# Performance work log

Hardware: AMD Instinct MI355X
Metric: run time of the kernel (lower is better)

Reference implementation:

```python
import jax, jax.numpy as jnp
import numpy as np

LAYERS = [3, 256, 256, 256, 256, 256, 256, 3]
W_BC, W_DIV, W_JXB = 1.0, 1.0, 1.0  # weight1 = [1.0, 1.0, 1.0]


def setup_inputs() -> dict:
    key = jax.random.key(0)
    ks = jax.random.split(key, 32)
    N0, NF = 16384, 32768
    inp = {
        "x0": jax.random.uniform(ks[0], (N0, 1), jnp.float32),
        "y0": jax.random.uniform(ks[1], (N0, 1), jnp.float32),
        "bx0": jax.random.normal(ks[2], (N0, 1), jnp.float32),
        "by0": jax.random.normal(ks[3], (N0, 1), jnp.float32),
        "bz0": jax.random.normal(ks[4], (N0, 1), jnp.float32),
        "xyz_f": jax.random.uniform(ks[5], (NF, 3), jnp.float32),
        "lb": jnp.zeros((3,), jnp.float32),
        "ub": jnp.ones((3,), jnp.float32),
    }
    # Xavier-normal weights, zero biases (as in initialize_NN)
    for l in range(len(LAYERS) - 1):
        fan_in, fan_out = LAYERS[l], LAYERS[l + 1]
        std = (2.0 / (fan_in + fan_out)) ** 0.5
        inp[f"W{l}"] = std * jax.random.normal(ks[6 + l], (fan_in, fan_out), jnp.float32)
        inp[f"b{l}"] = jnp.zeros((1, fan_out), jnp.float32)
    return inp


def reference(x0, y0, bx0, by0, bz0, xyz_f, lb, ub,
              W0, b0, W1, b1, W2, b2, W3, b3, W4, b4, W5, b5, W6, b6):
    Ws = [W0, W1, W2, W3, W4, W5, W6]
    bs = [b0, b1, b2, b3, b4, b5, b6]

    def net(p):  # p: (3,) -> (3,) field [bx, by, bz]
        h = 2.0 * (p - lb) / (ub - lb) - 1.0
        for W, b in zip(Ws[:-1], bs[:-1]):
            h = jnp.tanh(h @ W + b[0])
        return h @ Ws[-1] + bs[-1][0]

    # Boundary term at z = 0
    pts0 = jnp.concatenate([x0, y0, jnp.zeros_like(x0)], axis=1)  # (N0, 3)
    b_bc = jax.vmap(net)(pts0)  # (N0, 3)

    # One fused forward-mode pass gives the full 3x3 Jacobian + primal,
    # replacing the 9 separate autograd.grad sweeps of the torch code.
    def val_and_jac(p):
        primal, jac = jax.vmap(lambda t: jax.jvp(net, (p,), (t,)))(jnp.eye(3, dtype=p.dtype))
        return primal[0], jac  # jac[j, i] = d b_i / d x_j

    bf, jac = jax.vmap(val_and_jac)(xyz_f)  # (NF, 3), (NF, 3, 3)

    div = jac[:, 0, 0] + jac[:, 1, 1] + jac[:, 2, 2]  # bx_x + by_y + bz_z
    bx, by, bz = bf[:, 0], bf[:, 1], bf[:, 2]
    jx = jac[:, 1, 2] - jac[:, 2, 1]  # bz_y - by_z
    jy = jac[:, 2, 0] - jac[:, 0, 2]  # bx_z - bz_x
    jz = jac[:, 0, 1] - jac[:, 1, 0]  # by_x - bx_y
    jxb = (jy * bz - jz * by) ** 2 + (jz * bx - jx * bz) ** 2 + (jx * by - jy * bx) ** 2

    loss = (W_BC * jnp.mean((b_bc[:, 0:1] - bx0) ** 2)
            + W_BC * jnp.mean((b_bc[:, 1:2] - by0) ** 2)
            + W_BC * jnp.mean((b_bc[:, 2:3] - bz0) ** 2)
            + W_DIV * jnp.mean(div ** 2)
            + W_JXB * jnp.mean(jxb))
    return loss
```

## Files before the change

### kernel.cpp

```cpp
#include <hip/hip_runtime.h>
#include <math.h>

typedef short bf16x8 __attribute__((ext_vector_type(8)));
typedef float f32x4 __attribute__((ext_vector_type(4)));

#define NPT0 16384
#define NPTF 32768

__device__ __forceinline__ short f2b(float f) {
  union { float f; unsigned u; } v; v.f = f;
  return (short)((v.u + 0x7FFFu + ((v.u >> 16) & 1u)) >> 16);
}
__device__ __forceinline__ int cvtpk(float a, float b) {
  int r;
  asm("v_cvt_pk_bf16_f32 %0, %1, %2" : "=v"(r) : "v"(a), "v"(b));
  return r;
}
__device__ __forceinline__ float tanh_fast(float z) {
  const float e = __expf(2.f * z);
  return 1.f - 2.f * __builtin_amdgcn_rcpf(e + 1.f);
}
__device__ __forceinline__ int inplane(int n, int c) {
  return ((n >> 5) << 9) + ((((n >> 3) & 3) * 16 + c) << 3) + (n & 7);
}

__global__ void prep_kernel(const float* __restrict__ W1, const float* __restrict__ W2,
                            const float* __restrict__ W3, const float* __restrict__ W4,
                            const float* __restrict__ W5, const float* __restrict__ W6,
                            short* __restrict__ Wt)
{
  const int i = blockIdx.x * 256 + threadIdx.x;
  if (i < 5 * 65536) {
    const int layer = i >> 16;
    const float* src = layer == 0 ? W1 : layer == 1 ? W2 : layer == 2 ? W3
                     : layer == 3 ? W4 : W5;
    const int w  = i & 65535;
    const int nt = w >> 12;
    const int ks = (w >> 9) & 7;
    const int l  = (w >> 3) & 63;
    const int e  = w & 7;
    const int n  = nt * 16 + (l & 15);
    const int k  = ks * 32 + (l >> 4) * 8 + e;
    Wt[i] = f2b(src[k * 256 + n]);
  } else {
    const int w  = i - 5 * 65536;
    const int ks = w >> 9;
    const int l  = (w >> 3) & 63;
    const int e  = w & 7;
    const int n  = l & 15;
    const int k  = ks * 32 + (l >> 4) * 8 + e;
    Wt[i] = (n < 3) ? f2b(W6[k * 3 + n]) : (short)0;
  }
}

__global__ __launch_bounds__(512, 4) void field_kernel(
    const float* __restrict__ xyz_f,
    const float* __restrict__ lb, const float* __restrict__ ub,
    const float* __restrict__ W0, const float* __restrict__ b0,
    const float* __restrict__ b1, const float* __restrict__ b2,
    const float* __restrict__ b3, const float* __restrict__ b4,
    const float* __restrict__ b5,
    const short* __restrict__ Wt,
    const float* __restrict__ b6,
    float* __restrict__ part_div2, float* __restrict__ part_jxb)
{
  __shared__ short act[4 * 8192];
  __shared__ float redD[4 * 96];
  const int tid = threadIdx.x;
  const int lane = tid & 63;
  const int wv = tid >> 6;
  const int c = lane & 15;
  const int kg = lane >> 4;

  const float lbx = lb[0], lby = lb[1], lbz = lb[2];
  const float sx = 2.f / (ub[0] - lbx);
  const float sy = 2.f / (ub[1] - lby);
  const float sz = 2.f / (ub[2] - lbz);

  {
    const int pp = tid & 15;
    const int pg = (tid >> 4) & 1;
    const int pt = blockIdx.x * 32 + pg * 16 + pp;
    const int n0 = (tid >> 5) * 16;
    const float hx = (xyz_f[pt * 3 + 0] - lbx) * sx - 1.f;
    const float hy = (xyz_f[pt * 3 + 1] - lby) * sy - 1.f;
    const float hz = (xyz_f[pt * 3 + 2] - lbz) * sz - 1.f;
    float th[16], vx[16], vy[16], vz[16];
#pragma unroll
    for (int j = 0; j < 16; ++j) {
      const int n = n0 + j;
      const float w0 = W0[n], w1 = W0[256 + n], w2 = W0[512 + n];
      const float z = b0[n] + hx * w0 + hy * w1 + hz * w2;
      const float t = tanh_fast(z);
      const float g = 1.f - t * t;
      th[j] = t;
      vx[j] = g * sx * w0;
      vy[j] = g * sy * w1;
      vz[j] = g * sz * w2;
    }
    const int ks0 = n0 >> 5;
    const int kgb = (n0 >> 3) & 3;
#pragma unroll
    for (int half = 0; half < 2; ++half) {
      const int j0 = half * 8;
      const int idx = pg * 4096 + ks0 * 512 + ((kgb + half) * 16 + pp) * 8;
      int4 o0, o1, o2, o3;
      o0.x = cvtpk(th[j0+0], th[j0+1]); o0.y = cvtpk(th[j0+2], th[j0+3]);
      o0.z = cvtpk(th[j0+4], th[j0+5]); o0.w = cvtpk(th[j0+6], th[j0+7]);
      o1.x = cvtpk(vx[j0+0], vx[j0+1]); o1.y = cvtpk(vx[j0+2], vx[j0+3]);
      o1.z = cvtpk(vx[j0+4], vx[j0+5]); o1.w = cvtpk(vx[j0+6], vx[j0+7]);
      o2.x = cvtpk(vy[j0+0], vy[j0+1]); o2.y = cvtpk(vy[j0+2], vy[j0+3]);
      o2.z = cvtpk(vy[j0+4], vy[j0+5]); o2.w = cvtpk(vy[j0+6], vy[j0+7]);
      o3.x = cvtpk(vz[j0+0], vz[j0+1]); o3.y = cvtpk(vz[j0+2], vz[j0+3]);
      o3.z = cvtpk(vz[j0+4], vz[j0+5]); o3.w = cvtpk(vz[j0+6], vz[j0+7]);
      *(int4*)&act[idx]          = o0;
      *(int4*)&act[8192 + idx]   = o1;
      *(int4*)&act[16384 + idx]  = o2;
      *(int4*)&act[24576 + idx]  = o3;
    }
  }
  __syncthreads();

  const float* const bsArr[5] = {b1, b2, b3, b4, b5};

#pragma unroll
  for (int layer = 0; layer < 5; ++layer) {
    const short* wbase = Wt + layer * 65536 + (wv * 2) * 4096 + lane * 8;

    f32x4 acc[2][4][2];
#pragma unroll
    for (int t = 0; t < 2; ++t)
#pragma unroll
      for (int s = 0; s < 4; ++s)
#pragma unroll
        for (int g = 0; g < 2; ++g) acc[t][s][g] = (f32x4){0.f, 0.f, 0.f, 0.f};

#pragma unroll
    for (int ks = 0; ks < 8; ++ks) {
      const int sa = ks * 512 + lane * 8;
      const bf16x8 w0 = *(const bf16x8*)(wbase + ks * 512);
      const bf16x8 w1 = *(const bf16x8*)(wbase + 4096 + ks * 512);
#pragma unroll
      for (int g = 0; g < 2; ++g) {
        const bf16x8 a0 = *(const bf16x8*)&act[g * 4096 + sa];
        const bf16x8 a1 = *(const bf16x8*)&act[8192 + g * 4096 + sa];
        const bf16x8 a2 = *(const bf16x8*)&act[16384 + g * 4096 + sa];
        const bf16x8 a3 = *(const bf16x8*)&act[24576 + g * 4096 + sa];
        acc[0][0][g] = __builtin_amdgcn_mfma_f32_16x16x32_bf16(w0, a0, acc[0][0][g], 0, 0, 0);
        acc[0][1][g] = __builtin_amdgcn_mfma_f32_16x16x32_bf16(w0, a1, acc[0][1][g], 0, 0, 0);
        acc[0][2][g] = __builtin_amdgcn_mfma_f32_16x16x32_bf16(w0, a2, acc[0][2][g], 0, 0, 0);
        acc[0][3][g] = __builtin_amdgcn_mfma_f32_16x16x32_bf16(w0, a3, acc[0][3][g], 0, 0, 0);
        acc[1][0][g] = __builtin_amdgcn_mfma_f32_16x16x32_bf16(w1, a0, acc[1][0][g], 0, 0, 0);
        acc[1][1][g] = __builtin_amdgcn_mfma_f32_16x16x32_bf16(w1, a1, acc[1][1][g], 0, 0, 0);
        acc[1][2][g] = __builtin_amdgcn_mfma_f32_16x16x32_bf16(w1, a2, acc[1][2][g], 0, 0, 0);
        acc[1][3][g] = __builtin_amdgcn_mfma_f32_16x16x32_bf16(w1, a3, acc[1][3][g], 0, 0, 0);
      }
    }
    __syncthreads();

    const float* bl = bsArr[layer];
#pragma unroll
    for (int t = 0; t < 2; ++t) {
      const int n0 = (wv * 2 + t) * 16 + kg * 4;
      const f32x4 bias = *(const f32x4*)(bl + n0);
#pragma unroll
      for (int g = 0; g < 2; ++g) {
        float th[4], gd[4];
#pragma unroll
        for (int r = 0; r < 4; ++r) {
          th[r] = tanh_fast(acc[t][0][g][r] + bias[r]);
          gd[r] = 1.f - th[r] * th[r];
        }
        int2 o0, o1, o2, o3;
        o0.x = cvtpk(th[0], th[1]);
        o0.y = cvtpk(th[2], th[3]);
        o1.x = cvtpk(gd[0] * acc[t][1][g][0], gd[1] * acc[t][1][g][1]);
        o1.y = cvtpk(gd[2] * acc[t][1][g][2], gd[3] * acc[t][1][g][3]);
        o2.x = cvtpk(gd[0] * acc[t][2][g][0], gd[1] * acc[t][2][g][1]);
        o2.y = cvtpk(gd[2] * acc[t][2][g][2], gd[3] * acc[t][2][g][3]);
        o3.x = cvtpk(gd[0] * acc[t][3][g][0], gd[1] * acc[t][3][g][1]);
        o3.y = cvtpk(gd[2] * acc[t][3][g][2], gd[3] * acc[t][3][g][3]);
        const int idx = g * 4096 + inplane(n0, c);
        *(int2*)&act[idx]          = o0;
        *(int2*)&act[8192 + idx]   = o1;
        *(int2*)&act[16384 + idx]  = o2;
        *(int2*)&act[24576 + idx]  = o3;
      }
    }
    __syncthreads();
  }

  {
    const int s = wv >> 1, g = wv & 1;
    const short* w6 = Wt + 5 * 65536 + lane * 8;
    f32x4 accT = (f32x4){0.f, 0.f, 0.f, 0.f};
#pragma unroll
    for (int ks = 0; ks < 8; ++ks) {
      const bf16x8 w = *(const bf16x8*)(w6 + ks * 512);
      const bf16x8 b = *(const bf16x8*)&act[s * 8192 + g * 4096 + ks * 512 + lane * 8];
      accT = __builtin_amdgcn_mfma_f32_16x16x32_bf16(w, b, accT, 0, 0, 0);
    }
    if (kg == 0) {
      redD[s * 96 + 0  + g * 16 + c] = accT[0];
      redD[s * 96 + 32 + g * 16 + c] = accT[1];
      redD[s * 96 + 64 + g * 16 + c] = accT[2];
    }
  }
  __syncthreads();
  if (tid < 32) {
    const int p = tid;
    const float bx = redD[0 + p]   + b6[0];
    const float by = redD[32 + p]  + b6[1];
    const float bz = redD[64 + p]  + b6[2];
    const float j00 = redD[96 + p],  j01 = redD[128 + p], j02 = redD[160 + p];
    const float j10 = redD[192 + p], j11 = redD[224 + p], j12 = redD[256 + p];
    const float j20 = redD[288 + p], j21 = redD[320 + p], j22 = redD[352 + p];
    const float dv = j00 + j11 + j22;
    const float jx = j12 - j21;
    const float jy = j20 - j02;
    const float jz = j01 - j10;
    const float e1 = jy * bz - jz * by;
    const float e2 = jz * bx - jx * bz;
    const float e3 = jx * by - jy * bx;
    float d2 = dv * dv;
    float jb = e1 * e1 + e2 * e2 + e3 * e3;
#pragma unroll
    for (int m = 1; m < 32; m <<= 1) {
      d2 += __shfl_xor(d2, m);
      jb += __shfl_xor(jb, m);
    }
    if (tid == 0) {
      part_div2[blockIdx.x] = d2;
      part_jxb[blockIdx.x]  = jb;
    }
  }
}

__global__ __launch_bounds__(512, 4) void bc_kernel(
    const float* __restrict__ x0, const float* __restrict__ y0,
    const float* __restrict__ bx0, const float* __restrict__ by0,
    const float* __restrict__ bz0,
    const float* __restrict__ lb, const float* __restrict__ ub,
    const float* __restrict__ W0, const float* __restrict__ b0,
    const float* __restrict__ b1, const float* __restrict__ b2,
    const float* __restrict__ b3, const float* __restrict__ b4,
    const float* __restrict__ b5,
    const short* __restrict__ Wt,
    const float* __restrict__ b6,
    float* __restrict__ part_bc)
{
  __shared__ short act[8192];
  __shared__ float red[2];
  const int tid = threadIdx.x;
  const int lane = tid & 63;
  const int wv = tid >> 6;
  const int c = lane & 15;
  const int kg = lane >> 4;

  const float lbx = lb[0], lby = lb[1], lbz = lb[2];
  const float sx = 2.f / (ub[0] - lbx);
  const float sy = 2.f / (ub[1] - lby);
  const float sz = 2.f / (ub[2] - lbz);

  {
    const int pp = tid & 15;
    const int pg = (tid >> 4) & 1;
    const int pt = blockIdx.x * 32 + pg * 16 + pp;
    const int n0 = (tid >> 5) * 16;
    const float hx = (x0[pt] - lbx) * sx - 1.f;
    const float hy = (y0[pt] - lby) * sy - 1.f;
    const float hz = (0.f - lbz) * sz - 1.f;
    float th[16];
#pragma unroll
    for (int j = 0; j < 16; ++j) {
      const int n = n0 + j;
      const float z = b0[n] + hx * W0[n] + hy * W0[256 + n] + hz * W0[512 + n];
      th[j] = tanh_fast(z);
    }
    const int ks0 = n0 >> 5;
    const int kgb = (n0 >> 3) & 3;
#pragma unroll
    for (int half = 0; half < 2; ++half) {
      const int j0 = half * 8;
      int4 o;
      o.x = cvtpk(th[j0+0], th[j0+1]); o.y = cvtpk(th[j0+2], th[j0+3]);
      o.z = cvtpk(th[j0+4], th[j0+5]); o.w = cvtpk(th[j0+6], th[j0+7]);
      *(int4*)&act[pg * 4096 + ks0 * 512 + ((kgb + half) * 16 + pp) * 8] = o;
    }
  }
  __syncthreads();

  const float* const bsArr[5] = {b1, b2, b3, b4, b5};

#pragma unroll
  for (int layer = 0; layer < 5; ++layer) {
    const short* wbase = Wt + layer * 65536 + (wv * 2) * 4096 + lane * 8;

    bf16x8 a[2][8];
#pragma unroll
    for (int g = 0; g < 2; ++g)
#pragma unroll
      for (int ks = 0; ks < 8; ++ks)
        a[g][ks] = *(const bf16x8*)&act[g * 4096 + ks * 512 + lane * 8];
    __syncthreads();

    f32x4 acc[2][2];
#pragma unroll
    for (int t = 0; t < 2; ++t)
#pragma unroll
      for (int g = 0; g < 2; ++g) acc[t][g] = (f32x4){0.f, 0.f, 0.f, 0.f};

#pragma unroll
    for (int ks = 0; ks < 8; ++ks) {
      const bf16x8 w0 = *(const bf16x8*)(wbase + ks * 512);
      const bf16x8 w1 = *(const bf16x8*)(wbase + 4096 + ks * 512);
      acc[0][0] = __builtin_amdgcn_mfma_f32_16x16x32_bf16(w0, a[0][ks], acc[0][0], 0, 0, 0);
      acc[0][1] = __builtin_amdgcn_mfma_f32_16x16x32_bf16(w0, a[1][ks], acc[0][1], 0, 0, 0);
      acc[1][0] = __builtin_amdgcn_mfma_f32_16x16x32_bf16(w1, a[0][ks], acc[1][0], 0, 0, 0);
      acc[1][1] = __builtin_amdgcn_mfma_f32_16x16x32_bf16(w1, a[1][ks], acc[1][1], 0, 0, 0);
    }

    const float* bl = bsArr[layer];
#pragma unroll
    for (int t = 0; t < 2; ++t) {
      const int n0 = (wv * 2 + t) * 16 + kg * 4;
      const f32x4 bias = *(const f32x4*)(bl + n0);
#pragma unroll
      for (int g = 0; g < 2; ++g) {
        float th[4];
#pragma unroll
        for (int r = 0; r < 4; ++r) th[r] = tanh_fast(acc[t][g][r] + bias[r]);
        int2 o;
        o.x = cvtpk(th[0], th[1]);
        o.y = cvtpk(th[2], th[3]);
        *(int2*)&act[g * 4096 + inplane(n0, c)] = o;
      }
    }
    __syncthreads();
  }

  if (wv < 2) {
    const int g = wv;
    const short* w6 = Wt + 5 * 65536 + lane * 8;
    f32x4 accT = (f32x4){0.f, 0.f, 0.f, 0.f};
#pragma unroll
    for (int ks = 0; ks < 8; ++ks) {
      const bf16x8 w = *(const bf16x8*)(w6 + ks * 512);
      const bf16x8 b = *(const bf16x8*)&act[g * 4096 + ks * 512 + lane * 8];
      accT = __builtin_amdgcn_mfma_f32_16x16x32_bf16(w, b, accT, 0, 0, 0);
    }
    if (lane < 16) {
      const int pt = blockIdx.x * 32 + g * 16 + lane;
      const float ex = accT[0] + b6[0] - bx0[pt];
      const float ey = accT[1] + b6[1] - by0[pt];
      const float ez = accT[2] + b6[2] - bz0[pt];
      float abc = ex * ex + ey * ey + ez * ez;
#pragma unroll
      for (int m = 1; m < 16; m <<= 1) abc += __shfl_xor(abc, m);
      if (lane == 0) red[g] = abc;
    }
  }
  __syncthreads();
  if (tid == 0) part_bc[blockIdx.x] = red[0] + red[1];
}

__global__ void reduce_kernel(const float* __restrict__ parts, float* __restrict__ out)
{
  __shared__ float sdata[12];
  const int tid = threadIdx.x, lane = tid & 63, wv = tid >> 6;
  float d = 0.f, j = 0.f, b = 0.f;
  for (int i = tid; i < 1024; i += 256) { d += parts[i]; j += parts[1024 + i]; }
  for (int i = tid; i < 512; i += 256) b += parts[2048 + i];
  for (int off = 32; off > 0; off >>= 1) {
    d += __shfl_down(d, off);
    j += __shfl_down(j, off);
    b += __shfl_down(b, off);
  }
  if (lane == 0) {
    sdata[wv * 3 + 0] = d;
    sdata[wv * 3 + 1] = j;
    sdata[wv * 3 + 2] = b;
  }
  __syncthreads();
  if (tid == 0) {
    float sd = 0.f, sj = 0.f, sb = 0.f;
    for (int w = 0; w < 4; ++w) {
      sd += sdata[w * 3 + 0];
      sj += sdata[w * 3 + 1];
      sb += sdata[w * 3 + 2];
    }
    out[0] = sb / (float)NPT0 + sd / (float)NPTF + sj / (float)NPTF;
  }
}

extern "C" void kernel_launch(void* const* d_in, const int* in_sizes, int n_in,
                              void* d_out, int out_size, void* d_ws, size_t ws_size,
                              hipStream_t stream)
{
  const float* x0    = (const float*)d_in[0];
  const float* y0    = (const float*)d_in[1];
  const float* bx0   = (const float*)d_in[2];
  const float* by0   = (const float*)d_in[3];
  const float* bz0   = (const float*)d_in[4];
  const float* xyz_f = (const float*)d_in[5];
  const float* lb    = (const float*)d_in[6];
  const float* ub    = (const float*)d_in[7];
  const float* W0 = (const float*)d_in[8];
  const float* b0 = (const float*)d_in[9];
  const float* W1 = (const float*)d_in[10];
  const float* b1 = (const float*)d_in[11];
  const float* W2 = (const float*)d_in[12];
  const float* b2 = (const float*)d_in[13];
  const float* W3 = (const float*)d_in[14];
  const float* b3 = (const float*)d_in[15];
  const float* W4 = (const float*)d_in[16];
  const float* b4 = (const float*)d_in[17];
  const float* W5 = (const float*)d_in[18];
  const float* b5 = (const float*)d_in[19];
  const float* W6 = (const float*)d_in[20];
  const float* b6 = (const float*)d_in[21];

  short* Wt = (short*)d_ws;
  float* parts = (float*)((char*)d_ws + (5 * 65536 + 4096) * sizeof(short));
  float* p_div2 = parts;
  float* p_jxb  = parts + 1024;
  float* p_bc   = parts + 2048;

  prep_kernel<<<1296, 256, 0, stream>>>(W1, W2, W3, W4, W5, W6, Wt);
  field_kernel<<<1024, 512, 0, stream>>>(xyz_f, lb, ub, W0, b0,
      b1, b2, b3, b4, b5, Wt, b6, p_div2, p_jxb);
  bc_kernel<<<512, 512, 0, stream>>>(x0, y0, bx0, by0, bz0, lb, ub, W0, b0,
      b1, b2, b3, b4, b5, Wt, b6, p_bc);
  reduce_kernel<<<1, 256, 0, stream>>>(parts, (float*)d_out);
}
```

Measured before the change: 106.9 us.

## Split waves into value/tangent roles sharing weights across four output tiles

Reorganizes the per-layer MFMA work so each pair of waves covers 64 output neurons. One wave of the pair handles the primal and x-tangent streams and the other handles the y and z tangents, instead of each wave covering 32 neurons for all four streams. Each wave now loads four weight fragments and two activation planes per k-step, where before it loaded two weight fragments and four planes. This changes the ratio of global weight loads to LDS activation reads. The epilogue is split so role-0 waves compute tanh and store the derivative gd in an extra LDS region, then role-1 waves read gd back after a barrier. This costs an added __syncthreads per layer and serializes the epilogue across roles.

```diff
diff --git a/kernel.cpp b/kernel.cpp
--- a/kernel.cpp
+++ b/kernel.cpp
@@ -64,13 +64,15 @@
     const float* __restrict__ b6,
     float* __restrict__ part_div2, float* __restrict__ part_jxb)
 {
-  __shared__ short act[4 * 8192];
-  __shared__ float redD[4 * 96];
+  __shared__ alignas(16) short act[40960];
+  float* redD = (float*)&act[32768];
   const int tid = threadIdx.x;
   const int lane = tid & 63;
   const int wv = tid >> 6;
   const int c = lane & 15;
   const int kg = lane >> 4;
+  const int set = wv >> 1;
+  const int role = wv & 1;
 
   const float lbx = lb[0], lby = lb[1], lbz = lb[2];
   const float sx = 2.f / (ub[0] - lbx);
@@ -122,69 +124,88 @@
   __syncthreads();
 
   const float* const bsArr[5] = {b1, b2, b3, b4, b5};
+  const int sb = role * 2;
 
 #pragma unroll
   for (int layer = 0; layer < 5; ++layer) {
-    const short* wbase = Wt + layer * 65536 + (wv * 2) * 4096 + lane * 8;
-
-    f32x4 acc[2][4][2];
-#pragma unroll
-    for (int t = 0; t < 2; ++t)
-#pragma unroll
-      for (int s = 0; s < 4; ++s)
+    const short* wbase = Wt + layer * 65536 + (set * 4) * 4096 + lane * 8;
+
+    f32x4 acc[4][2][2];
+#pragma unroll
+    for (int t = 0; t < 4; ++t)
+#pragma unroll
+      for (int s = 0; s < 2; ++s)
 #pragma unroll
         for (int g = 0; g < 2; ++g) acc[t][s][g] = (f32x4){0.f, 0.f, 0.f, 0.f};
 
 #pragma unroll
     for (int ks = 0; ks < 8; ++ks) {
       const int sa = ks * 512 + lane * 8;
-      const bf16x8 w0 = *(const bf16x8*)(wbase + ks * 512);
-      const bf16x8 w1 = *(const bf16x8*)(wbase + 4096 + ks * 512);
-#pragma unroll
-      for (int g = 0; g < 2; ++g) {
-        const bf16x8 a0 = *(const bf16x8*)&act[g * 4096 + sa];
-        const bf16x8 a1 = *(const bf16x8*)&act[8192 + g * 4096 + sa];
-        const bf16x8 a2 = *(const bf16x8*)&act[16384 + g * 4096 + sa];
-        const bf16x8 a3 = *(const bf16x8*)&act[24576 + g * 4096 + sa];
-        acc[0][0][g] = __builtin_amdgcn_mfma_f32_16x16x32_bf16(w0, a0, acc[0][0][g], 0, 0, 0);
-        acc[0][1][g] = __builtin_amdgcn_mfma_f32_16x16x32_bf16(w0, a1, acc[0][1][g], 0, 0, 0);
-        acc[0][2][g] = __builtin_amdgcn_mfma_f32_16x16x32_bf16(w0, a2, acc[0][2][g], 0, 0, 0);
-        acc[0][3][g] = __builtin_amdgcn_mfma_f32_16x16x32_bf16(w0, a3, acc[0][3][g], 0, 0, 0);
-        acc[1][0][g] = __builtin_amdgcn_mfma_f32_16x16x32_bf16(w1, a0, acc[1][0][g], 0, 0, 0);
-        acc[1][1][g] = __builtin_amdgcn_mfma_f32_16x16x32_bf16(w1, a1, acc[1][1][g], 0, 0, 0);
-        acc[1][2][g] = __builtin_amdgcn_mfma_f32_16x16x32_bf16(w1, a2, acc[1][2][g], 0, 0, 0);
-        acc[1][3][g] = __builtin_amdgcn_mfma_f32_16x16x32_bf16(w1, a3, acc[1][3][g], 0, 0, 0);
+      const bf16x8 a00 = *(const bf16x8*)&act[(sb * 2 + 0) * 4096 + sa];
+      const bf16x8 a01 = *(const bf16x8*)&act[(sb * 2 + 1) * 4096 + sa];
+      const bf16x8 a10 = *(const bf16x8*)&act[(sb * 2 + 2) * 4096 + sa];
+      const bf16x8 a11 = *(const bf16x8*)&act[(sb * 2 + 3) * 4096 + sa];
+#pragma unroll
+      for (int t = 0; t < 4; ++t) {
+        const bf16x8 w = *(const bf16x8*)(wbase + t * 4096 + ks * 512);
+        acc[t][0][0] = __builtin_amdgcn_mfma_f32_16x16x32_bf16(w, a00, acc[t][0][0], 0, 0, 0);
+        acc[t][0][1] = __builtin_amdgcn_mfma_f32_16x16x32_bf16(w, a01, acc[t][0][1], 0, 0, 0);
+        acc[t][1][0] = __builtin_amdgcn_mfma_f32_16x16x32_bf16(w, a10, acc[t][1][0], 0, 0, 0);
+        acc[t][1][1] = __builtin_amdgcn_mfma_f32_16x16x32_bf16(w, a11, acc[t][1][1], 0, 0, 0);
       }
     }
     __syncthreads();
 
-    const float* bl = bsArr[layer];
-#pragma unroll
-    for (int t = 0; t < 2; ++t) {
-      const int n0 = (wv * 2 + t) * 16 + kg * 4;
-      const f32x4 bias = *(const f32x4*)(bl + n0);
-#pragma unroll
-      for (int g = 0; g < 2; ++g) {
-        float th[4], gd[4];
-#pragma unroll
-        for (int r = 0; r < 4; ++r) {
-          th[r] = tanh_fast(acc[t][0][g][r] + bias[r]);
-          gd[r] = 1.f - th[r] * th[r];
+    if (role == 0) {
+      const float* bl = bsArr[layer];
+#pragma unroll
+      for (int t = 0; t < 4; ++t) {
+        const int n0 = (set * 4 + t) * 16 + kg * 4;
+        const f32x4 bias = *(const f32x4*)(bl + n0);
+        const int idx = inplane(n0, c);
+#pragma unroll
+        for (int g = 0; g < 2; ++g) {
+          float th[4], gd[4];
+#pragma unroll
+          for (int r = 0; r < 4; ++r) {
+            th[r] = tanh_fast(acc[t][0][g][r] + bias[r]);
+            gd[r] = 1.f - th[r] * th[r];
+          }
+          int2 o0, o1, og;
+          o0.x = cvtpk(th[0], th[1]);
+          o0.y = cvtpk(th[2], th[3]);
+          o1.x = cvtpk(gd[0] * acc[t][1][g][0], gd[1] * acc[t][1][g][1]);
+          o1.y = cvtpk(gd[2] * acc[t][1][g][2], gd[3] * acc[t][1][g][3]);
+          og.x = cvtpk(gd[0], gd[1]);
+          og.y = cvtpk(gd[2], gd[3]);
+          *(int2*)&act[g * 4096 + idx]           = o0;
+          *(int2*)&act[(2 + g) * 4096 + idx]     = o1;
+          *(int2*)&act[32768 + g * 4096 + idx]   = og;
         }
-        int2 o0, o1, o2, o3;
-        o0.x = cvtpk(th[0], th[1]);
-        o0.y = cvtpk(th[2], th[3]);
-        o1.x = cvtpk(gd[0] * acc[t][1][g][0], gd[1] * acc[t][1][g][1]);
-        o1.y = cvtpk(gd[2] * acc[t][1][g][2], gd[3] * acc[t][1][g][3]);
-        o2.x = cvtpk(gd[0] * acc[t][2][g][0], gd[1] * acc[t][2][g][1]);
-        o2.y = cvtpk(gd[2] * acc[t][2][g][2], gd[3] * acc[t][2][g][3]);
-        o3.x = cvtpk(gd[0] * acc[t][3][g][0], gd[1] * acc[t][3][g][1]);
-        o3.y = cvtpk(gd[2] * acc[t][3][g][2], gd[3] * acc[t][3][g][3]);
-        const int idx = g * 4096 + inplane(n0, c);
-        *(int2*)&act[idx]          = o0;
-        *(int2*)&act[8192 + idx]   = o1;
-        *(int2*)&act[16384 + idx]  = o2;
-        *(int2*)&act[24576 + idx]  = o3;
+      }
+    }
+    __syncthreads();
+
+    if (role == 1) {
+#pragma unroll
+      for (int t = 0; t < 4; ++t) {
+        const int n0 = (set * 4 + t) * 16 + kg * 4;
+        const int idx = inplane(n0, c);
+#pragma unroll
+        for (int g = 0; g < 2; ++g) {
+          const int2 og = *(const int2*)&act[32768 + g * 4096 + idx];
+          const float gd0 = __uint_as_float(((unsigned)og.x) << 16);
+          const float gd1 = __uint_as_float(((unsigned)og.x) & 0xffff0000u);
+          const float gd2 = __uint_as_float(((unsigned)og.y) << 16);
+          const float gd3 = __uint_as_float(((unsigned)og.y) & 0xffff0000u);
+          int2 o2, o3;
+          o2.x = cvtpk(gd0 * acc[t][0][g][0], gd1 * acc[t][0][g][1]);
+          o2.y = cvtpk(gd2 * acc[t][0][g][2], gd3 * acc[t][0][g][3]);
+          o3.x = cvtpk(gd0 * acc[t][1][g][0], gd1 * acc[t][1][g][1]);
+          o3.y = cvtpk(gd2 * acc[t][1][g][2], gd3 * acc[t][1][g][3]);
+          *(int2*)&act[(4 + g) * 4096 + idx] = o2;
+          *(int2*)&act[(6 + g) * 4096 + idx] = o3;
+        }
       }
     }
     __syncthreads();
@@ -197,7 +218,7 @@
 #pragma unroll
     for (int ks = 0; ks < 8; ++ks) {
       const bf16x8 w = *(const bf16x8*)(w6 + ks * 512);
-      const bf16x8 b = *(const bf16x8*)&act[s * 8192 + g * 4096 + ks * 512 + lane * 8];
+      const bf16x8 b = *(const bf16x8*)&act[(s * 2 + g) * 4096 + ks * 512 + lane * 8];
       accT = __builtin_amdgcn_mfma_f32_16x16x32_bf16(w, b, accT, 0, 0, 0);
     }
     if (kg == 0) {
```

New measurement: 128.7 us. 20.4% more time.

## Halve field kernel block to 4 waves, each computing 4 output tiles

Applied to the files above, without the earlier changes.

The field kernel now runs 256 threads per block instead of 512. Each wave covers four 16-column output tiles instead of two, so every activation fragment it reads from LDS feeds four weight tiles rather than two, which cuts LDS read traffic per MFMA. The first-layer setup and the final output layer are remapped to the smaller thread count. In exchange each wave holds twice as many accumulators, raising register pressure, and there are fewer waves per block to hide latency.

```diff
diff --git a/kernel.cpp b/kernel.cpp
--- a/kernel.cpp
+++ b/kernel.cpp
@@ -53,7 +53,7 @@
   }
 }
 
-__global__ __launch_bounds__(512, 4) void field_kernel(
+__global__ __launch_bounds__(256, 2) void field_kernel(
     const float* __restrict__ xyz_f,
     const float* __restrict__ lb, const float* __restrict__ ub,
     const float* __restrict__ W0, const float* __restrict__ b0,
@@ -78,45 +78,49 @@
   const float sz = 2.f / (ub[2] - lbz);
 
   {
-    const int pp = tid & 15;
-    const int pg = (tid >> 4) & 1;
+    const int p = tid >> 3;
+    const int pp = p & 15;
+    const int pg = p >> 4;
     const int pt = blockIdx.x * 32 + pg * 16 + pp;
-    const int n0 = (tid >> 5) * 16;
     const float hx = (xyz_f[pt * 3 + 0] - lbx) * sx - 1.f;
     const float hy = (xyz_f[pt * 3 + 1] - lby) * sy - 1.f;
     const float hz = (xyz_f[pt * 3 + 2] - lbz) * sz - 1.f;
-    float th[16], vx[16], vy[16], vz[16];
-#pragma unroll
-    for (int j = 0; j < 16; ++j) {
-      const int n = n0 + j;
-      const float w0 = W0[n], w1 = W0[256 + n], w2 = W0[512 + n];
-      const float z = b0[n] + hx * w0 + hy * w1 + hz * w2;
-      const float t = tanh_fast(z);
-      const float g = 1.f - t * t;
-      th[j] = t;
-      vx[j] = g * sx * w0;
-      vy[j] = g * sy * w1;
-      vz[j] = g * sz * w2;
-    }
-    const int ks0 = n0 >> 5;
-    const int kgb = (n0 >> 3) & 3;
-#pragma unroll
-    for (int half = 0; half < 2; ++half) {
-      const int j0 = half * 8;
-      const int idx = pg * 4096 + ks0 * 512 + ((kgb + half) * 16 + pp) * 8;
-      int4 o0, o1, o2, o3;
-      o0.x = cvtpk(th[j0+0], th[j0+1]); o0.y = cvtpk(th[j0+2], th[j0+3]);
-      o0.z = cvtpk(th[j0+4], th[j0+5]); o0.w = cvtpk(th[j0+6], th[j0+7]);
-      o1.x = cvtpk(vx[j0+0], vx[j0+1]); o1.y = cvtpk(vx[j0+2], vx[j0+3]);
-      o1.z = cvtpk(vx[j0+4], vx[j0+5]); o1.w = cvtpk(vx[j0+6], vx[j0+7]);
-      o2.x = cvtpk(vy[j0+0], vy[j0+1]); o2.y = cvtpk(vy[j0+2], vy[j0+3]);
-      o2.z = cvtpk(vy[j0+4], vy[j0+5]); o2.w = cvtpk(vy[j0+6], vy[j0+7]);
-      o3.x = cvtpk(vz[j0+0], vz[j0+1]); o3.y = cvtpk(vz[j0+2], vz[j0+3]);
-      o3.z = cvtpk(vz[j0+4], vz[j0+5]); o3.w = cvtpk(vz[j0+6], vz[j0+7]);
-      *(int4*)&act[idx]          = o0;
-      *(int4*)&act[8192 + idx]   = o1;
-      *(int4*)&act[16384 + idx]  = o2;
-      *(int4*)&act[24576 + idx]  = o3;
+#pragma unroll
+    for (int h16 = 0; h16 < 2; ++h16) {
+      const int n0 = (tid & 7) * 32 + h16 * 16;
+      float th[16], vx[16], vy[16], vz[16];
+#pragma unroll
+      for (int j = 0; j < 16; ++j) {
+        const int n = n0 + j;
+        const float w0 = W0[n], w1 = W0[256 + n], w2 = W0[512 + n];
+        const float z = b0[n] + hx * w0 + hy * w1 + hz * w2;
+        const float t = tanh_fast(z);
+        const float g = 1.f - t * t;
+        th[j] = t;
+        vx[j] = g * sx * w0;
+        vy[j] = g * sy * w1;
+        vz[j] = g * sz * w2;
+      }
+      const int ks0 = n0 >> 5;
+      const int kgb = (n0 >> 3) & 3;
+#pragma unroll
+      for (int half = 0; half < 2; ++half) {
+        const int j0 = half * 8;
+        const int idx = pg * 4096 + ks0 * 512 + ((kgb + half) * 16 + pp) * 8;
+        int4 o0, o1, o2, o3;
+        o0.x = cvtpk(th[j0+0], th[j0+1]); o0.y = cvtpk(th[j0+2], th[j0+3]);
+        o0.z = cvtpk(th[j0+4], th[j0+5]); o0.w = cvtpk(th[j0+6], th[j0+7]);
+        o1.x = cvtpk(vx[j0+0], vx[j0+1]); o1.y = cvtpk(vx[j0+2], vx[j0+3]);
+        o1.z = cvtpk(vx[j0+4], vx[j0+5]); o1.w = cvtpk(vx[j0+6], vx[j0+7]);
+        o2.x = cvtpk(vy[j0+0], vy[j0+1]); o2.y = cvtpk(vy[j0+2], vy[j0+3]);
+        o2.z = cvtpk(vy[j0+4], vy[j0+5]); o2.w = cvtpk(vy[j0+6], vy[j0+7]);
+        o3.x = cvtpk(vz[j0+0], vz[j0+1]); o3.y = cvtpk(vz[j0+2], vz[j0+3]);
+        o3.z = cvtpk(vz[j0+4], vz[j0+5]); o3.w = cvtpk(vz[j0+6], vz[j0+7]);
+        *(int4*)&act[idx]          = o0;
+        *(int4*)&act[8192 + idx]   = o1;
+        *(int4*)&act[16384 + idx]  = o2;
+        *(int4*)&act[24576 + idx]  = o3;
+      }
     }
   }
   __syncthreads();
@@ -125,11 +129,11 @@
 
 #pragma unroll
   for (int layer = 0; layer < 5; ++layer) {
-    const short* wbase = Wt + layer * 65536 + (wv * 2) * 4096 + lane * 8;
-
-    f32x4 acc[2][4][2];
-#pragma unroll
-    for (int t = 0; t < 2; ++t)
+    const short* wbase = Wt + layer * 65536 + (wv * 4) * 4096 + lane * 8;
+
+    f32x4 acc[4][4][2];
+#pragma unroll
+    for (int t = 0; t < 4; ++t)
 #pragma unroll
       for (int s = 0; s < 4; ++s)
 #pragma unroll
@@ -138,31 +142,30 @@
 #pragma unroll
     for (int ks = 0; ks < 8; ++ks) {
       const int sa = ks * 512 + lane * 8;
-      const bf16x8 w0 = *(const bf16x8*)(wbase + ks * 512);
-      const bf16x8 w1 = *(const bf16x8*)(wbase + 4096 + ks * 512);
-#pragma unroll
-      for (int g = 0; g < 2; ++g) {
-        const bf16x8 a0 = *(const bf16x8*)&act[g * 4096 + sa];
-        const bf16x8 a1 = *(const bf16x8*)&act[8192 + g * 4096 + sa];
-        const bf16x8 a2 = *(const bf16x8*)&act[16384 + g * 4096 + sa];
-        const bf16x8 a3 = *(const bf16x8*)&act[24576 + g * 4096 + sa];
-        acc[0][0][g] = __builtin_amdgcn_mfma_f32_16x16x32_bf16(w0, a0, acc[0][0][g], 0, 0, 0);
-        acc[0][1][g] = __builtin_amdgcn_mfma_f32_16x16x32_bf16(w0, a1, acc[0][1][g], 0, 0, 0);
-        acc[0][2][g] = __builtin_amdgcn_mfma_f32_16x16x32_bf16(w0, a2, acc[0][2][g], 0, 0, 0);
-        acc[0][3][g] = __builtin_amdgcn_mfma_f32_16x16x32_bf16(w0, a3, acc[0][3][g], 0, 0, 0);
-        acc[1][0][g] = __builtin_amdgcn_mfma_f32_16x16x32_bf16(w1, a0, acc[1][0][g], 0, 0, 0);
-        acc[1][1][g] = __builtin_amdgcn_mfma_f32_16x16x32_bf16(w1, a1, acc[1][1][g], 0, 0, 0);
-        acc[1][2][g] = __builtin_amdgcn_mfma_f32_16x16x32_bf16(w1, a2, acc[1][2][g], 0, 0, 0);
-        acc[1][3][g] = __builtin_amdgcn_mfma_f32_16x16x32_bf16(w1, a3, acc[1][3][g], 0, 0, 0);
+      bf16x8 a[4][2];
+#pragma unroll
+      for (int s = 0; s < 4; ++s)
+#pragma unroll
+        for (int g = 0; g < 2; ++g)
+          a[s][g] = *(const bf16x8*)&act[s * 8192 + g * 4096 + sa];
+#pragma unroll
+      for (int t = 0; t < 4; ++t) {
+        const bf16x8 w = *(const bf16x8*)(wbase + t * 4096 + ks * 512);
+#pragma unroll
+        for (int s = 0; s < 4; ++s) {
+          acc[t][s][0] = __builtin_amdgcn_mfma_f32_16x16x32_bf16(w, a[s][0], acc[t][s][0], 0, 0, 0);
+          acc[t][s][1] = __builtin_amdgcn_mfma_f32_16x16x32_bf16(w, a[s][1], acc[t][s][1], 0, 0, 0);
+        }
       }
     }
     __syncthreads();
 
     const float* bl = bsArr[layer];
 #pragma unroll
-    for (int t = 0; t < 2; ++t) {
-      const int n0 = (wv * 2 + t) * 16 + kg * 4;
+    for (int t = 0; t < 4; ++t) {
+      const int n0 = (wv * 4 + t) * 16 + kg * 4;
       const f32x4 bias = *(const f32x4*)(bl + n0);
+      const int idxb = inplane(n0, c);
 #pragma unroll
       for (int g = 0; g < 2; ++g) {
         float th[4], gd[4];
@@ -180,7 +183,7 @@
         o2.y = cvtpk(gd[2] * acc[t][2][g][2], gd[3] * acc[t][2][g][3]);
         o3.x = cvtpk(gd[0] * acc[t][3][g][0], gd[1] * acc[t][3][g][1]);
         o3.y = cvtpk(gd[2] * acc[t][3][g][2], gd[3] * acc[t][3][g][3]);
-        const int idx = g * 4096 + inplane(n0, c);
+        const int idx = g * 4096 + idxb;
         *(int2*)&act[idx]          = o0;
         *(int2*)&act[8192 + idx]   = o1;
         *(int2*)&act[16384 + idx]  = o2;
@@ -191,19 +194,25 @@
   }
 
   {
-    const int s = wv >> 1, g = wv & 1;
     const short* w6 = Wt + 5 * 65536 + lane * 8;
-    f32x4 accT = (f32x4){0.f, 0.f, 0.f, 0.f};
+    f32x4 accT0 = (f32x4){0.f, 0.f, 0.f, 0.f};
+    f32x4 accT1 = (f32x4){0.f, 0.f, 0.f, 0.f};
 #pragma unroll
     for (int ks = 0; ks < 8; ++ks) {
       const bf16x8 w = *(const bf16x8*)(w6 + ks * 512);
-      const bf16x8 b = *(const bf16x8*)&act[s * 8192 + g * 4096 + ks * 512 + lane * 8];
-      accT = __builtin_amdgcn_mfma_f32_16x16x32_bf16(w, b, accT, 0, 0, 0);
+      const int sa = ks * 512 + lane * 8;
+      const bf16x8 bA = *(const bf16x8*)&act[wv * 8192 + sa];
+      const bf16x8 bB = *(const bf16x8*)&act[wv * 8192 + 4096 + sa];
+      accT0 = __builtin_amdgcn_mfma_f32_16x16x32_bf16(w, bA, accT0, 0, 0, 0);
+      accT1 = __builtin_amdgcn_mfma_f32_16x16x32_bf16(w, bB, accT1, 0, 0, 0);
     }
     if (kg == 0) {
-      redD[s * 96 + 0  + g * 16 + c] = accT[0];
-      redD[s * 96 + 32 + g * 16 + c] = accT[1];
-      redD[s * 96 + 64 + g * 16 + c] = accT[2];
+      redD[wv * 96 + 0  + 0 * 16 + c] = accT0[0];
+      redD[wv * 96 + 32 + 0 * 16 + c] = accT0[1];
+      redD[wv * 96 + 64 + 0 * 16 + c] = accT0[2];
+      redD[wv * 96 + 0  + 1 * 16 + c] = accT1[0];
+      redD[wv * 96 + 32 + 1 * 16 + c] = accT1[1];
+      redD[wv * 96 + 64 + 1 * 16 + c] = accT1[2];
     }
   }
   __syncthreads();
@@ -427,7 +436,7 @@
   float* p_bc   = parts + 2048;
 
   prep_kernel<<<1296, 256, 0, stream>>>(W1, W2, W3, W4, W5, W6, Wt);
-  field_kernel<<<1024, 512, 0, stream>>>(xyz_f, lb, ub, W0, b0,
+  field_kernel<<<1024, 256, 0, stream>>>(xyz_f, lb, ub, W0, b0,
       b1, b2, b3, b4, b5, Wt, b6, p_div2, p_jxb);
   bc_kernel<<<512, 512, 0, stream>>>(x0, y0, bx0, by0, bz0, lb, ub, W0, b0,
       b1, b2, b3, b4, b5, Wt, b6, p_bc);
```

After: 132.8 us. +24.2%, slower.
